# Performance work log

Measured on AMD Instinct MI355X. Metric: run time of the kernel, lower is better.

## Reference

```python
import jax, jax.numpy as jnp
import numpy as np

D_MODEL = 1024
D_KV = 64
N_HEADS = 16
INNER = N_HEADS * D_KV
EPS = 1e-6


def setup_inputs() -> dict:
    key = jax.random.key(0)
    ks = jax.random.split(key, 8)
    B, SQ, SKV = 2, 2048, 4096
    hidden_states = jax.random.normal(ks[0], (B, SQ, D_MODEL), dtype=jnp.float32)
    key_value_states = jax.random.normal(ks[1], (B, SKV, D_MODEL), dtype=jnp.float32)
    attention_mask = jnp.zeros((B, 1, 1, SKV), dtype=jnp.float32)
    # nn.Linear(in, out, bias=False): y = x @ W.T; store W as [in, out] here
    s = 0.02
    Wq = jax.random.normal(ks[2], (D_MODEL, INNER), dtype=jnp.float32) * s
    Wk = jax.random.normal(ks[3], (D_MODEL, INNER), dtype=jnp.float32) * s
    Wv = jax.random.normal(ks[4], (D_MODEL, INNER), dtype=jnp.float32) * s
    Wo = jax.random.normal(ks[5], (INNER, D_MODEL), dtype=jnp.float32) * s
    ln_weight = jnp.ones((D_MODEL,), dtype=jnp.float32)
    return {
        "hidden_states": hidden_states,
        "key_value_states": key_value_states,
        "attention_mask": attention_mask,
        "ln_weight": ln_weight,
        "Wq": Wq,
        "Wk": Wk,
        "Wv": Wv,
        "Wo": Wo,
    }


def _t5_rmsnorm(x, w, eps=EPS):
    # no mean subtraction, variance in fp32
    var = jnp.mean(jnp.square(x.astype(jnp.float32)), axis=-1, keepdims=True)
    return w * (x * jax.lax.rsqrt(var + eps)).astype(x.dtype)


def reference(hidden_states, key_value_states, attention_mask, ln_weight, Wq, Wk, Wv, Wo):
    B, SQ, _ = hidden_states.shape
    SKV = key_value_states.shape[1]
    normed = _t5_rmsnorm(hidden_states, ln_weight)

    # projections -> [B, H, S, Dk]
    q = (normed @ Wq).reshape(B, SQ, N_HEADS, D_KV).transpose(0, 2, 1, 3)
    k = (key_value_states @ Wk).reshape(B, SKV, N_HEADS, D_KV).transpose(0, 2, 1, 3)
    v = (key_value_states @ Wv).reshape(B, SKV, N_HEADS, D_KV).transpose(0, 2, 1, 3)

    # T5: NO 1/sqrt(d) scaling
    scores = jnp.einsum("bhqd,bhkd->bhqk", q, k) + attention_mask
    attn = jax.nn.softmax(scores.astype(jnp.float32), axis=-1).astype(scores.dtype)
    ctx = jnp.einsum("bhqk,bhkd->bhqd", attn, v)
    ctx = ctx.transpose(0, 2, 1, 3).reshape(B, SQ, INNER)
    attn_out = ctx @ Wo
    return hidden_states + attn_out
```

## Files before the change

kernel.cpp:

```cpp
#include <hip/hip_runtime.h>

typedef unsigned short u16;
typedef unsigned int u32;
typedef __attribute__((ext_vector_type(4))) float f32x4;
typedef __attribute__((ext_vector_type(8))) short short8;

#define BB   2
#define SQL  2048
#define SKVL 4096
#define DM   1024
#define NH   16
#define DK   64
#define L2E  1.44269504f

#if __has_builtin(__builtin_amdgcn_exp2f)
#define EXP2(x) __builtin_amdgcn_exp2f(x)
#else
#define EXP2(x) exp2f(x)
#endif

__device__ __forceinline__ u16 f2bf(float f) {
  union { float f; unsigned u; } v; v.f = f;
  unsigned r = v.u + 0x7fff + ((v.u >> 16) & 1);
  return (u16)(r >> 16);
}

__device__ __forceinline__ void gload16(const void* g, void* lds) {
  __builtin_amdgcn_global_load_lds(
      (const __attribute__((address_space(1))) unsigned int*)g,
      (__attribute__((address_space(3))) unsigned int*)lds, 16, 0, 0);
}

__global__ void rmsnorm_kernel(const float* __restrict__ x, const float* __restrict__ w,
                               u16* __restrict__ out) {
  int row = blockIdx.x;
  int t = threadIdx.x;
  float4 v = ((const float4*)(x + (size_t)row * DM))[t];
  float ss = v.x * v.x + v.y * v.y + v.z * v.z + v.w * v.w;
#pragma unroll
  for (int m = 32; m >= 1; m >>= 1) ss += __shfl_xor(ss, m, 64);
  __shared__ float red[4];
  int lane = t & 63, wv = t >> 6;
  if (lane == 0) red[wv] = ss;
  __syncthreads();
  float total = red[0] + red[1] + red[2] + red[3];
  float scale = rsqrtf(total * (1.0f / DM) + 1e-6f);
  float4 g = ((const float4*)w)[t];
  ushort4 o;
  o.x = f2bf(v.x * scale * g.x);
  o.y = f2bf(v.y * scale * g.y);
  o.z = f2bf(v.z * scale * g.z);
  o.w = f2bf(v.w * scale * g.w);
  ((ushort4*)(out + (size_t)row * DM))[t] = o;
}

__global__ void cvt_kernel(const float* __restrict__ in, u16* __restrict__ out) {
  int i = blockIdx.x * 256 + threadIdx.x;
  float4 v = ((const float4*)in)[i];
  ushort4 o;
  o.x = f2bf(v.x); o.y = f2bf(v.y); o.z = f2bf(v.z); o.w = f2bf(v.w);
  ((ushort4*)out)[i] = o;
}

__global__ void tcvt_kernel(const float* __restrict__ W, u16* __restrict__ Wt) {
  __shared__ float tile[32][33];
  int tx = threadIdx.x & 31, ty = threadIdx.x >> 5;
  int k0 = blockIdx.y * 32, n0 = blockIdx.x * 32;
#pragma unroll
  for (int i = 0; i < 4; i++)
    tile[ty + i * 8][tx] = W[(size_t)(k0 + ty + i * 8) * DM + n0 + tx];
  __syncthreads();
#pragma unroll
  for (int i = 0; i < 4; i++)
    Wt[(size_t)(n0 + ty + i * 8) * DM + k0 + tx] = f2bf(tile[tx][ty + i * 8]);
}

template <int MODE>
__global__ void gemm_kernel(const u16* __restrict__ A, const u16* __restrict__ Bt,
                            void* __restrict__ C, void* __restrict__ C2,
                            const float* __restrict__ aux, int N, float scale) {
  const int K = 1024;
  __shared__ __align__(16) u16 Al[128 * 32];
  __shared__ __align__(16) u16 Bl[128 * 32];
  int tid = threadIdx.x, lane = tid & 63, w = tid >> 6;
  int l15 = lane & 15, quad = lane >> 4;
  int wy = w >> 1, wx = w & 1;
  int tm = blockIdx.x * 128, tn = blockIdx.y * 128;
  f32x4 acc[4][4] = {};

  for (int k0 = 0; k0 < K; k0 += 32) {
    __syncthreads();
#pragma unroll
    for (int r = 0; r < 2; r++) {
      int mg = w * 2 + r;
      gload16(A + (size_t)(tm + mg * 16 + l15) * K + k0 + quad * 8, &Al[mg * 512]);
      gload16(Bt + (size_t)(tn + mg * 16 + l15) * K + k0 + quad * 8, &Bl[mg * 512]);
    }
    __syncthreads();
    short8 af[4], bfr[4];
#pragma unroll
    for (int i = 0; i < 4; i++) {
      af[i] = *(const short8*)&Al[((wy * 4 + i) * 64 + lane) * 8];
      bfr[i] = *(const short8*)&Bl[((wx * 4 + i) * 64 + lane) * 8];
    }
#pragma unroll
    for (int mt = 0; mt < 4; mt++)
#pragma unroll
      for (int nt = 0; nt < 4; nt++)
        acc[mt][nt] = __builtin_amdgcn_mfma_f32_16x16x32_bf16(af[mt], bfr[nt], acc[mt][nt], 0, 0, 0);
  }

#pragma unroll
  for (int mt = 0; mt < 4; mt++) {
    int m0 = tm + wy * 64 + mt * 16 + quad * 4;
#pragma unroll
    for (int nt = 0; nt < 4; nt++) {
      int n = tn + wx * 64 + nt * 16 + l15;
      if (MODE == 0) {
#pragma unroll
        for (int r = 0; r < 4; r++)
          ((u16*)C)[(size_t)(m0 + r) * N + n] = f2bf(acc[mt][nt][r] * scale);
      } else if (MODE == 2) {
#pragma unroll
        for (int r = 0; r < 4; r++) {
          size_t idx = (size_t)(m0 + r) * N + n;
          ((float*)C)[idx] = aux[idx] + acc[mt][nt][r];
        }
      } else {
        if (tn < 1024) {
#pragma unroll
          for (int r = 0; r < 4; r++)
            ((u16*)C)[(size_t)(m0 + r) * 1024 + n] = f2bf(acc[mt][nt][r]);
        } else {
          int nv = n - 1024;
          int h = nv >> 6, d = nv & 63;
          int b = m0 >> 12, skv = m0 & 4095;
          float4 mv = *(const float4*)(aux + (size_t)b * SKVL + skv);
          ushort4 o;
          o.x = f2bf(acc[mt][nt][0] * EXP2(mv.x * L2E));
          o.y = f2bf(acc[mt][nt][1] * EXP2(mv.y * L2E));
          o.z = f2bf(acc[mt][nt][2] * EXP2(mv.z * L2E));
          o.w = f2bf(acc[mt][nt][3] * EXP2(mv.w * L2E));
          *(ushort4*)((u16*)C2 + (size_t)((b * NH + h) * DK + d) * SKVL + skv) = o;
        }
      }
    }
  }
}

#define MFMA(a, b, c) __builtin_amdgcn_mfma_f32_16x16x32_bf16(a, b, c, 0, 0, 0)

__global__ __launch_bounds__(256, 2) void flash_kernel(
    const u16* __restrict__ Qp, const u16* __restrict__ Kp, const u16* __restrict__ Vtp,
    const float* __restrict__ mask, u16* __restrict__ ctx) {
  __shared__ __align__(16) u16 Kl[64 * 64];
  __shared__ __align__(16) u16 Vl[64 * 64];
  __shared__ __align__(16) u16 Pl[4][2048];
  __shared__ __align__(16) u16 pml[SKVL];

  int tid = threadIdx.x, lane = tid & 63, w = tid >> 6;
  int l15 = lane & 15, quad = lane >> 4;
  int qb = blockIdx.x, bh = blockIdx.y;
  int b = bh >> 4, h = bh & 15;
  int q0 = qb * 128 + w * 32;

  {
    int i0 = tid * 16;
#pragma unroll
    for (int g = 0; g < 4; g++) {
      float4 mv = *(const float4*)(mask + (size_t)b * SKVL + i0 + g * 4);
      ushort4 o;
      o.x = f2bf(EXP2(mv.x * L2E)); o.y = f2bf(EXP2(mv.y * L2E));
      o.z = f2bf(EXP2(mv.z * L2E)); o.w = f2bf(EXP2(mv.w * L2E));
      *(ushort4*)&pml[i0 + g * 4] = o;
    }
  }

  short8 qf[2][2];
#pragma unroll
  for (int mt = 0; mt < 2; mt++)
#pragma unroll
    for (int kf = 0; kf < 2; kf++)
      qf[mt][kf] = *(const short8*)(Qp + (size_t)(b * SQL + q0 + mt * 16 + l15) * DM +
                                    h * DK + kf * 32 + quad * 8);

  f32x4 of[2][4] = {};
  f32x4 la[2] = {};
  const int pbase = (quad >> 1) * 256 + (quad & 1) * 8 + l15 * 16;
  char* plw = (char*)&Pl[w][0];

  for (int kv0 = 0; kv0 < SKVL; kv0 += 64) {
    __syncthreads();
    {
#pragma unroll
      for (int r = 0; r < 2; r++) {
        int g = w * 2 + r;
        int kt = g >> 1, kf = g & 1;
        gload16(Kp + (size_t)(b * SKVL + kv0 + kt * 16 + l15) * DM + h * DK + kf * 32 + quad * 8,
                &Kl[g * 512]);
        gload16(Vtp + (size_t)((b * NH + h) * DK + kt * 16 + l15) * SKVL + kv0 + kf * 32 + quad * 8,
                &Vl[g * 512]);
      }
    }
    __syncthreads();

#pragma unroll
    for (int kt = 0; kt < 4; kt++) {
      short8 k0 = *(const short8*)&Kl[((kt * 2 + 0) * 64 + lane) * 8];
      short8 k1 = *(const short8*)&Kl[((kt * 2 + 1) * 64 + lane) * 8];
#pragma unroll
      for (int mt = 0; mt < 2; mt++) {
        f32x4 st = {0.f, 0.f, 0.f, 0.f};
        st = MFMA(k0, qf[mt][0], st);
        st = MFMA(k1, qf[mt][1], st);
        union { float f; u32 u; } c0, c1, c2, c3;
        c0.f = EXP2(st[0]); c1.f = EXP2(st[1]);
        c2.f = EXP2(st[2]); c3.f = EXP2(st[3]);
        uint2 pk;
        pk.x = ((c0.u + 0x8000u) >> 16) | ((c1.u + 0x8000u) & 0xffff0000u);
        pk.y = ((c2.u + 0x8000u) >> 16) | ((c3.u + 0x8000u) & 0xffff0000u);
        *(uint2*)(plw + mt * 2048 + kt * 512 + pbase) = pk;
      }
    }
    asm volatile("s_waitcnt lgkmcnt(0)" ::: "memory");

#pragma unroll
    for (int kf = 0; kf < 2; kf++) {
      short8 pmf = *(const short8*)&pml[kv0 + kf * 32 + quad * 8];
      short8 pa0 = *(const short8*)(plw + ((0 * 2 + kf) * 4 + quad) * 256 + l15 * 16);
      short8 pa1 = *(const short8*)(plw + ((1 * 2 + kf) * 4 + quad) * 256 + l15 * 16);
      la[0] = MFMA(pa0, pmf, la[0]);
      la[1] = MFMA(pa1, pmf, la[1]);
#pragma unroll
      for (int nt = 0; nt < 4; nt++) {
        short8 vf = *(const short8*)&Vl[((nt * 2 + kf) * 64 + lane) * 8];
        of[0][nt] = MFMA(pa0, vf, of[0][nt]);
        of[1][nt] = MFMA(pa1, vf, of[1][nt]);
      }
    }
  }

#pragma unroll
  for (int mt = 0; mt < 2; mt++)
#pragma unroll
    for (int r = 0; r < 4; r++) {
      float inv = 1.0f / la[mt][r];
      int q = q0 + mt * 16 + quad * 4 + r;
#pragma unroll
      for (int nt = 0; nt < 4; nt++) {
        int d = nt * 16 + l15;
        ctx[(size_t)(b * SQL + q) * DM + h * DK + d] = f2bf(of[mt][nt][r] * inv);
      }
    }
}

extern "C" void kernel_launch(void* const* d_in, const int* in_sizes, int n_in,
                              void* d_out, int out_size, void* d_ws, size_t ws_size,
                              hipStream_t stream) {
  const float* hidden = (const float*)d_in[0];
  const float* kvs    = (const float*)d_in[1];
  const float* mask   = (const float*)d_in[2];
  const float* lnw    = (const float*)d_in[3];
  const float* Wq     = (const float*)d_in[4];
  const float* Wk     = (const float*)d_in[5];
  const float* Wv     = (const float*)d_in[6];
  const float* Wo     = (const float*)d_in[7];
  char* ws = (char*)d_ws;

  u16* normed = (u16*)(ws + 0);
  u16* kvb    = (u16*)(ws + 8388608);
  u16* Wqt    = (u16*)(ws + 25165824);
  u16* Wkt    = (u16*)(ws + 27262976);
  u16* Wvt    = (u16*)(ws + 29360128);
  u16* Wot    = (u16*)(ws + 31457280);
  u16* Qb     = (u16*)(ws + 33554432);
  u16* Kbf    = (u16*)(ws + 41943040);
  u16* Vtb    = (u16*)(ws + 58720256);
  u16* ctxb   = (u16*)(ws + 75497472);

  rmsnorm_kernel<<<BB * SQL, 256, 0, stream>>>(hidden, lnw, normed);
  cvt_kernel<<<(BB * SKVL * DM) / 1024, 256, 0, stream>>>(kvs, kvb);
  dim3 tg(32, 32);
  tcvt_kernel<<<tg, 256, 0, stream>>>(Wq, Wqt);
  tcvt_kernel<<<tg, 256, 0, stream>>>(Wk, Wkt);
  tcvt_kernel<<<tg, 256, 0, stream>>>(Wv, Wvt);
  tcvt_kernel<<<tg, 256, 0, stream>>>(Wo, Wot);

  gemm_kernel<0><<<dim3(32, 8), 256, 0, stream>>>(normed, Wqt, Qb, nullptr, nullptr, 1024, L2E);
  gemm_kernel<3><<<dim3(64, 16), 256, 0, stream>>>(kvb, Wkt, Kbf, Vtb, mask, 2048, 1.0f);

  flash_kernel<<<dim3(SQL / 128, BB * NH), 256, 0, stream>>>(Qb, Kbf, Vtb, mask, ctxb);

  gemm_kernel<2><<<dim3(32, 8), 256, 0, stream>>>(ctxb, Wot, d_out, nullptr, hidden, 1024, 1.0f);
}
```

Measured before the change: 375.8 us.

## Split KV range across wave groups in flash kernel, fuse weight transposes, restructure V GEMM

The flash kernel now has each wave handle 64 query rows instead of 32. Two wave groups process alternate 64-key chunks of the KV sequence and combine their partial outputs and row sums through shared memory at the end. This doubles reuse of each K/V fragment per wave and halves the loop trip count, at the cost of more registers and 72KB of LDS, which may limit occupancy. The four weight transpose launches are merged into one grid launch. The V projection is computed as Wv^T·kv so the transposed V layout is written with row-contiguous stores instead of scattered 8-byte writes.

```diff
diff --git a/kernel.cpp b/kernel.cpp
--- a/kernel.cpp
+++ b/kernel.cpp
@@ -30,6 +30,8 @@
       (const __attribute__((address_space(1))) unsigned int*)g,
       (__attribute__((address_space(3))) unsigned int*)lds, 16, 0, 0);
 }
+
+#define MFMA(a, b, c) __builtin_amdgcn_mfma_f32_16x16x32_bf16(a, b, c, 0, 0, 0)
 
 __global__ void rmsnorm_kernel(const float* __restrict__ x, const float* __restrict__ w,
                                u16* __restrict__ out) {
@@ -62,7 +64,17 @@
   ((ushort4*)out)[i] = o;
 }
 
-__global__ void tcvt_kernel(const float* __restrict__ W, u16* __restrict__ Wt) {
+__global__ void tcvt4_kernel(const float* __restrict__ W0, const float* __restrict__ W1,
+                             const float* __restrict__ W2, const float* __restrict__ W3,
+                             u16* __restrict__ O0, u16* __restrict__ O1,
+                             u16* __restrict__ O2, u16* __restrict__ O3) {
+  const float* W; u16* Wt;
+  switch (blockIdx.z) {
+    case 0: W = W0; Wt = O0; break;
+    case 1: W = W1; Wt = O1; break;
+    case 2: W = W2; Wt = O2; break;
+    default: W = W3; Wt = O3; break;
+  }
   __shared__ float tile[32][33];
   int tx = threadIdx.x & 31, ty = threadIdx.x >> 5;
   int k0 = blockIdx.y * 32, n0 = blockIdx.x * 32;
@@ -77,8 +89,8 @@
 
 template <int MODE>
 __global__ void gemm_kernel(const u16* __restrict__ A, const u16* __restrict__ Bt,
-                            void* __restrict__ C, void* __restrict__ C2,
-                            const float* __restrict__ aux, int N, float scale) {
+                            void* __restrict__ C, const float* __restrict__ aux,
+                            int N, float scale) {
   const int K = 1024;
   __shared__ __align__(16) u16 Al[128 * 32];
   __shared__ __align__(16) u16 Bl[128 * 32];
@@ -107,7 +119,7 @@
     for (int mt = 0; mt < 4; mt++)
 #pragma unroll
       for (int nt = 0; nt < 4; nt++)
-        acc[mt][nt] = __builtin_amdgcn_mfma_f32_16x16x32_bf16(af[mt], bfr[nt], acc[mt][nt], 0, 0, 0);
+        acc[mt][nt] = MFMA(af[mt], bfr[nt], acc[mt][nt]);
   }
 
 #pragma unroll
@@ -120,49 +132,95 @@
 #pragma unroll
         for (int r = 0; r < 4; r++)
           ((u16*)C)[(size_t)(m0 + r) * N + n] = f2bf(acc[mt][nt][r] * scale);
-      } else if (MODE == 2) {
+      } else {
 #pragma unroll
         for (int r = 0; r < 4; r++) {
           size_t idx = (size_t)(m0 + r) * N + n;
           ((float*)C)[idx] = aux[idx] + acc[mt][nt][r];
         }
+      }
+    }
+  }
+}
+
+__global__ void kvgemm_kernel(const u16* __restrict__ kvb, const u16* __restrict__ Wkt,
+                              const u16* __restrict__ Wvt, u16* __restrict__ Kbf,
+                              u16* __restrict__ Vtb, const float* __restrict__ mask) {
+  const int K = 1024;
+  __shared__ __align__(16) u16 Al[128 * 32];
+  __shared__ __align__(16) u16 Bl[128 * 32];
+  int tid = threadIdx.x, lane = tid & 63, w = tid >> 6;
+  int l15 = lane & 15, quad = lane >> 4;
+  int wy = w >> 1, wx = w & 1;
+
+  int bid = blockIdx.x;
+  bool vmode = bid >= 512;
+  const u16 *A, *Bt;
+  int tm, tn;
+  if (!vmode) { A = kvb; Bt = Wkt; tm = (bid & 63) * 128; tn = (bid >> 6) * 128; }
+  else { int vid = bid - 512; A = Wvt; Bt = kvb; tm = (vid & 7) * 128; tn = (vid >> 3) * 128; }
+
+  f32x4 acc[4][4] = {};
+  for (int k0 = 0; k0 < K; k0 += 32) {
+    __syncthreads();
+#pragma unroll
+    for (int r = 0; r < 2; r++) {
+      int mg = w * 2 + r;
+      gload16(A + (size_t)(tm + mg * 16 + l15) * K + k0 + quad * 8, &Al[mg * 512]);
+      gload16(Bt + (size_t)(tn + mg * 16 + l15) * K + k0 + quad * 8, &Bl[mg * 512]);
+    }
+    __syncthreads();
+    short8 af[4], bfr[4];
+#pragma unroll
+    for (int i = 0; i < 4; i++) {
+      af[i] = *(const short8*)&Al[((wy * 4 + i) * 64 + lane) * 8];
+      bfr[i] = *(const short8*)&Bl[((wx * 4 + i) * 64 + lane) * 8];
+    }
+#pragma unroll
+    for (int mt = 0; mt < 4; mt++)
+#pragma unroll
+      for (int nt = 0; nt < 4; nt++)
+        acc[mt][nt] = MFMA(af[mt], bfr[nt], acc[mt][nt]);
+  }
+
+#pragma unroll
+  for (int mt = 0; mt < 4; mt++) {
+    int m0 = tm + wy * 64 + mt * 16 + quad * 4;
+#pragma unroll
+    for (int nt = 0; nt < 4; nt++) {
+      int n = tn + wx * 64 + nt * 16 + l15;
+      if (!vmode) {
+#pragma unroll
+        for (int r = 0; r < 4; r++)
+          Kbf[(size_t)(m0 + r) * 1024 + n] = f2bf(acc[mt][nt][r]);
       } else {
-        if (tn < 1024) {
-#pragma unroll
-          for (int r = 0; r < 4; r++)
-            ((u16*)C)[(size_t)(m0 + r) * 1024 + n] = f2bf(acc[mt][nt][r]);
-        } else {
-          int nv = n - 1024;
-          int h = nv >> 6, d = nv & 63;
-          int b = m0 >> 12, skv = m0 & 4095;
-          float4 mv = *(const float4*)(aux + (size_t)b * SKVL + skv);
-          ushort4 o;
-          o.x = f2bf(acc[mt][nt][0] * EXP2(mv.x * L2E));
-          o.y = f2bf(acc[mt][nt][1] * EXP2(mv.y * L2E));
-          o.z = f2bf(acc[mt][nt][2] * EXP2(mv.z * L2E));
-          o.w = f2bf(acc[mt][nt][3] * EXP2(mv.w * L2E));
-          *(ushort4*)((u16*)C2 + (size_t)((b * NH + h) * DK + d) * SKVL + skv) = o;
-        }
-      }
-    }
-  }
-}
-
-#define MFMA(a, b, c) __builtin_amdgcn_mfma_f32_16x16x32_bf16(a, b, c, 0, 0, 0)
+        float pm = EXP2(mask[n] * L2E);
+        int b = n >> 12, skv = n & 4095;
+#pragma unroll
+        for (int r = 0; r < 4; r++)
+          Vtb[((size_t)(b * 1024 + m0 + r) << 12) + skv] = f2bf(acc[mt][nt][r] * pm);
+      }
+    }
+  }
+}
 
 __global__ __launch_bounds__(256, 2) void flash_kernel(
     const u16* __restrict__ Qp, const u16* __restrict__ Kp, const u16* __restrict__ Vtp,
     const float* __restrict__ mask, u16* __restrict__ ctx) {
-  __shared__ __align__(16) u16 Kl[64 * 64];
-  __shared__ __align__(16) u16 Vl[64 * 64];
-  __shared__ __align__(16) u16 Pl[4][2048];
-  __shared__ __align__(16) u16 pml[SKVL];
+  __shared__ __align__(16) char smem[73728];
+  u16* Kl2 = (u16*)smem;
+  u16* Vl2 = (u16*)(smem + 16384);
+  char* pl_base = smem + 32768;
+  u16* pml = (u16*)(smem + 65536);
+  float* Ox = (float*)smem;
+  float* Ll = (float*)(smem + 32768);
 
   int tid = threadIdx.x, lane = tid & 63, w = tid >> 6;
   int l15 = lane & 15, quad = lane >> 4;
+  int grp = w >> 1, wg = w & 1;
   int qb = blockIdx.x, bh = blockIdx.y;
   int b = bh >> 4, h = bh & 15;
-  int q0 = qb * 128 + w * 32;
+  int q0 = qb * 128 + wg * 64;
 
   {
     int i0 = tid * 16;
@@ -176,40 +234,41 @@
     }
   }
 
-  short8 qf[2][2];
-#pragma unroll
-  for (int mt = 0; mt < 2; mt++)
+  short8 qf[4][2];
+#pragma unroll
+  for (int mt = 0; mt < 4; mt++)
 #pragma unroll
     for (int kf = 0; kf < 2; kf++)
       qf[mt][kf] = *(const short8*)(Qp + (size_t)(b * SQL + q0 + mt * 16 + l15) * DM +
                                     h * DK + kf * 32 + quad * 8);
 
-  f32x4 of[2][4] = {};
-  f32x4 la[2] = {};
+  f32x4 of[4][4] = {};
+  f32x4 la[4] = {};
+  char* plw = pl_base + w * 8192;
   const int pbase = (quad >> 1) * 256 + (quad & 1) * 8 + l15 * 16;
-  char* plw = (char*)&Pl[w][0];
-
-  for (int kv0 = 0; kv0 < SKVL; kv0 += 64) {
-    __syncthreads();
-    {
-#pragma unroll
-      for (int r = 0; r < 2; r++) {
-        int g = w * 2 + r;
-        int kt = g >> 1, kf = g & 1;
-        gload16(Kp + (size_t)(b * SKVL + kv0 + kt * 16 + l15) * DM + h * DK + kf * 32 + quad * 8,
-                &Kl[g * 512]);
-        gload16(Vtp + (size_t)((b * NH + h) * DK + kt * 16 + l15) * SKVL + kv0 + kf * 32 + quad * 8,
-                &Vl[g * 512]);
-      }
+  u16* Klg = Kl2 + grp * 4096;
+  u16* Vlg = Vl2 + grp * 4096;
+
+  for (int it = 0; it < 32; ++it) {
+    int kv0 = it * 128 + grp * 64;
+    __syncthreads();
+#pragma unroll
+    for (int r = 0; r < 4; r++) {
+      int u = wg * 4 + r;
+      int kt = u >> 1, kf = u & 1;
+      gload16(Kp + (size_t)(b * SKVL + kv0 + kt * 16 + l15) * DM + h * DK + kf * 32 + quad * 8,
+              &Klg[u * 512]);
+      gload16(Vtp + (size_t)((b * NH + h) * DK + kt * 16 + l15) * SKVL + kv0 + kf * 32 + quad * 8,
+              &Vlg[u * 512]);
     }
     __syncthreads();
 
 #pragma unroll
     for (int kt = 0; kt < 4; kt++) {
-      short8 k0 = *(const short8*)&Kl[((kt * 2 + 0) * 64 + lane) * 8];
-      short8 k1 = *(const short8*)&Kl[((kt * 2 + 1) * 64 + lane) * 8];
-#pragma unroll
-      for (int mt = 0; mt < 2; mt++) {
+      short8 k0 = *(const short8*)&Klg[((kt * 2 + 0) * 64 + lane) * 8];
+      short8 k1 = *(const short8*)&Klg[((kt * 2 + 1) * 64 + lane) * 8];
+#pragma unroll
+      for (int mt = 0; mt < 4; mt++) {
         f32x4 st = {0.f, 0.f, 0.f, 0.f};
         st = MFMA(k0, qf[mt][0], st);
         st = MFMA(k1, qf[mt][1], st);
@@ -227,31 +286,52 @@
 #pragma unroll
     for (int kf = 0; kf < 2; kf++) {
       short8 pmf = *(const short8*)&pml[kv0 + kf * 32 + quad * 8];
-      short8 pa0 = *(const short8*)(plw + ((0 * 2 + kf) * 4 + quad) * 256 + l15 * 16);
-      short8 pa1 = *(const short8*)(plw + ((1 * 2 + kf) * 4 + quad) * 256 + l15 * 16);
-      la[0] = MFMA(pa0, pmf, la[0]);
-      la[1] = MFMA(pa1, pmf, la[1]);
+      short8 pa[4];
+#pragma unroll
+      for (int mt = 0; mt < 4; mt++)
+        pa[mt] = *(const short8*)(plw + ((mt * 2 + kf) * 4 + quad) * 256 + l15 * 16);
+#pragma unroll
+      for (int mt = 0; mt < 4; mt++) la[mt] = MFMA(pa[mt], pmf, la[mt]);
 #pragma unroll
       for (int nt = 0; nt < 4; nt++) {
-        short8 vf = *(const short8*)&Vl[((nt * 2 + kf) * 64 + lane) * 8];
-        of[0][nt] = MFMA(pa0, vf, of[0][nt]);
-        of[1][nt] = MFMA(pa1, vf, of[1][nt]);
-      }
-    }
-  }
-
-#pragma unroll
-  for (int mt = 0; mt < 2; mt++)
-#pragma unroll
-    for (int r = 0; r < 4; r++) {
-      float inv = 1.0f / la[mt][r];
-      int q = q0 + mt * 16 + quad * 4 + r;
-#pragma unroll
-      for (int nt = 0; nt < 4; nt++) {
-        int d = nt * 16 + l15;
-        ctx[(size_t)(b * SQL + q) * DM + h * DK + d] = f2bf(of[mt][nt][r] * inv);
-      }
-    }
+        short8 vf = *(const short8*)&Vlg[((nt * 2 + kf) * 64 + lane) * 8];
+#pragma unroll
+        for (int mt = 0; mt < 4; mt++)
+          of[mt][nt] = MFMA(pa[mt], vf, of[mt][nt]);
+      }
+    }
+  }
+
+  __syncthreads();
+  if (grp == 1) {
+#pragma unroll
+    for (int mt = 0; mt < 4; mt++) {
+#pragma unroll
+      for (int nt = 0; nt < 4; nt++)
+#pragma unroll
+        for (int r = 0; r < 4; r++)
+          Ox[(wg * 64 + mt * 16 + quad * 4 + r) * 64 + nt * 16 + l15] = of[mt][nt][r];
+      if (l15 == 0)
+#pragma unroll
+        for (int r = 0; r < 4; r++) Ll[wg * 64 + mt * 16 + quad * 4 + r] = la[mt][r];
+    }
+  }
+  __syncthreads();
+  if (grp == 0) {
+#pragma unroll
+    for (int mt = 0; mt < 4; mt++)
+#pragma unroll
+      for (int r = 0; r < 4; r++) {
+        int ql = wg * 64 + mt * 16 + quad * 4 + r;
+        float inv = 1.0f / (la[mt][r] + Ll[ql]);
+        int q = qb * 128 + ql;
+#pragma unroll
+        for (int nt = 0; nt < 4; nt++) {
+          float ov = of[mt][nt][r] + Ox[ql * 64 + nt * 16 + l15];
+          ctx[(size_t)(b * SQL + q) * DM + h * DK + nt * 16 + l15] = f2bf(ov * inv);
+        }
+      }
+  }
 }
 
 extern "C" void kernel_launch(void* const* d_in, const int* in_sizes, int n_in,
@@ -280,16 +360,12 @@
 
   rmsnorm_kernel<<<BB * SQL, 256, 0, stream>>>(hidden, lnw, normed);
   cvt_kernel<<<(BB * SKVL * DM) / 1024, 256, 0, stream>>>(kvs, kvb);
-  dim3 tg(32, 32);
-  tcvt_kernel<<<tg, 256, 0, stream>>>(Wq, Wqt);
-  tcvt_kernel<<<tg, 256, 0, stream>>>(Wk, Wkt);
-  tcvt_kernel<<<tg, 256, 0, stream>>>(Wv, Wvt);
-  tcvt_kernel<<<tg, 256, 0, stream>>>(Wo, Wot);
-
-  gemm_kernel<0><<<dim3(32, 8), 256, 0, stream>>>(normed, Wqt, Qb, nullptr, nullptr, 1024, L2E);
-  gemm_kernel<3><<<dim3(64, 16), 256, 0, stream>>>(kvb, Wkt, Kbf, Vtb, mask, 2048, 1.0f);
+  tcvt4_kernel<<<dim3(32, 32, 4), 256, 0, stream>>>(Wq, Wk, Wv, Wo, Wqt, Wkt, Wvt, Wot);
+
+  gemm_kernel<0><<<dim3(32, 8), 256, 0, stream>>>(normed, Wqt, Qb, nullptr, 1024, L2E);
+  kvgemm_kernel<<<1024, 256, 0, stream>>>(kvb, Wkt, Wvt, Kbf, Vtb, mask);
 
   flash_kernel<<<dim3(SQL / 128, BB * NH), 256, 0, stream>>>(Qb, Kbf, Vtb, mask, ctxb);
 
-  gemm_kernel<2><<<dim3(32, 8), 256, 0, stream>>>(ctxb, Wot, d_out, nullptr, hidden, 1024, 1.0f);
-}
+  gemm_kernel<2><<<dim3(32, 8), 256, 0, stream>>>(ctxb, Wot, d_out, hidden, 1024, 1.0f);
+}
```

Result: faster. 350.9 us (-6.6%).
